# Kernel tuning notes

Measured on AMD Instinct MI355X. Metric: run time of the kernel, lower is better.

## Reference

```python
import jax, jax.numpy as jnp
import numpy as np

C = 768            # config.channels
CH, CW = 16, 16    # coarse span shape for group 'screen'
N = CH * CW        # total coarse positions = 256
FH, FW, FP = 16, 16, 2
F = FH * FW * FP   # fine_total = 512
K = 4              # top4 sample mode
B = 1024           # sb


def _ln(x, g, b, eps=1e-5):
    m = jnp.mean(x, axis=-1, keepdims=True)
    v = jnp.mean((x - m) ** 2, axis=-1, keepdims=True)
    return (x - m) / jnp.sqrt(v + eps) * g + b


def _mlp3(x, W1, b1, W2, b2, W3, b3):
    h = jax.nn.gelu(x @ W1 + b1)
    h = jax.nn.gelu(h @ W2 + b2)
    return h @ W3 + b3


def setup_inputs() -> dict:
    key = jax.random.key(0)
    ks = jax.random.split(key, 16)

    def w(k, fan_in, shape):
        return jax.random.normal(k, shape, jnp.float32) * (1.0 / np.sqrt(fan_in))

    return {
        "x": jax.random.normal(ks[0], (B, C), jnp.float32),
        "g_in": jnp.ones((C,), jnp.float32),
        "b_in": jnp.zeros((C,), jnp.float32),
        # coarse head: C -> C -> C -> N
        "cW1": w(ks[1], C, (C, C)), "cb1": jnp.zeros((C,), jnp.float32),
        "cW2": w(ks[2], C, (C, C)), "cb2": jnp.zeros((C,), jnp.float32),
        "cW3": w(ks[3], C, (C, N)), "cb3": jnp.zeros((N,), jnp.float32),
        # coarse embedding
        "emb": jax.random.normal(ks[4], (N, C), jnp.float32),
        "g_e": jnp.ones((C,), jnp.float32),
        "b_e": jnp.zeros((C,), jnp.float32),
        # fine head: 2C -> C -> C -> F
        "fW1": w(ks[5], 2 * C, (2 * C, C)), "fb1": jnp.zeros((C,), jnp.float32),
        "fW2": w(ks[6], C, (C, C)), "fb2": jnp.zeros((C,), jnp.float32),
        "fW3": w(ks[7], C, (C, F)), "fb3": jnp.zeros((F,), jnp.float32),
        # no-op head
        "nW": w(ks[8], C, (C, 1)), "nb": jnp.zeros((1,), jnp.float32),
    }


def reference(x, g_in, b_in, cW1, cb1, cW2, cb2, cW3, cb3, emb, g_e, b_e,
              fW1, fb1, fW2, fb2, fW3, fb3, nW, nb):
    b = x.shape[0]
    xn = _ln(x, g_in, b_in)                                   # (b, C)
    no_op = xn @ nW + nb                                      # (b, 1)
    coarse = _mlp3(xn, cW1, cb1, cW2, cb2, cW3, cb3)          # (b, N)

    # top4 routing
    _, i = jax.lax.top_k(coarse, K)                           # (b, K) int32
    e = _ln(emb[i], g_e, b_e)                                 # (b, K, C)
    fine_in = jnp.concatenate(
        [jnp.broadcast_to(xn[:, None, :], (b, K, C)), e], axis=-1)  # (b, K, 2C)
    fine = _mlp3(fine_in, fW1, fb1, fW2, fb2, fW3, fb3)       # (b, K, F)

    log_f = jnp.log(jnp.float32(F))
    xfull = jnp.broadcast_to(coarse[:, :, None], (b, N, F)) - log_f  # (b, N, F)
    upd = fine + log_f - jax.nn.logsumexp(fine, axis=-1, keepdims=True)
    xfull = xfull.at[jnp.arange(b)[:, None], i].add(upd)      # scatter-combine

    # per-group permute: (b, ch, cw, fh, fw, fp) -> (b, ch, fh, cw, fw, fp)
    xg = xfull.reshape(b, CH, CW, FH, FW, FP)
    xg = jnp.transpose(xg, (0, 1, 3, 2, 4, 5)).reshape(b, -1)
    return jnp.concatenate([no_op, xg], axis=-1)              # (b, 1 + N*F)
```

## Files before the change

### kernel.cpp

```cpp
#include <hip/hip_runtime.h>
#include <hip/hip_bf16.h>
#include <math.h>

typedef unsigned short u16;
typedef unsigned int   u32;
typedef __attribute__((ext_vector_type(8))) short s16x8;
typedef __attribute__((ext_vector_type(4))) float f32x4;

#define CB 768
#define NB 256
#define FB 512
#define BATCH 1024
#define OUTC 131073
#define LOGF 6.2383246250395077f

__device__ __forceinline__ u16 f2bf(float f){
    u32 u = __float_as_uint(f);
    u32 r = u + 0x7FFFu + ((u >> 16) & 1u);
    return (u16)(r >> 16);
}
__device__ __forceinline__ float bf2f(u16 s){ return __uint_as_float(((u32)s) << 16); }
__device__ __forceinline__ bool probe_bf(const void* g){ return ((const u16*)g)[0] == 0x3F80u; }
__device__ __forceinline__ float loadraw(const void* p, size_t i, bool isbf){
    return isbf ? bf2f(((const u16*)p)[i]) : ((const float*)p)[i];
}
__device__ __forceinline__ void split3(float f, u16& h, u16& l, u16& q){
    h = f2bf(f); float r1 = f - bf2f(h);
    l = f2bf(r1); float r2 = r1 - bf2f(l);
    q = f2bf(r2);
}
__device__ __forceinline__ float gelu_f(float x){
    return 0.5f * x * (1.0f + tanhf(0.7978845608028654f * (x + 0.044715f * x * x * x)));
}
__device__ __forceinline__ f32x4 mfma16x16x32(s16x8 a, s16x8 b, f32x4 c){
    return __builtin_amdgcn_mfma_f32_16x16x32_bf16(a, b, c, 0, 0, 0);
}

__device__ __forceinline__ float blockReduce(float v, float* sb, bool domax){
    #pragma unroll
    for (int o = 32; o > 0; o >>= 1){
        float ov = __shfl_down(v, o, 64);
        v = domax ? fmaxf(v, ov) : (v + ov);
    }
    int w = threadIdx.x >> 6, lane = threadIdx.x & 63;
    if (lane == 0) sb[w] = v;
    __syncthreads();
    float r = domax ? fmaxf(fmaxf(sb[0], sb[1]), fmaxf(sb[2], sb[3]))
                    : (sb[0] + sb[1] + sb[2] + sb[3]);
    __syncthreads();
    return r;
}

struct TransDesc { const void* src; u16* dh; u16* dl; int K; int N; int start; int tilesX; };
struct TD6 { TransDesc d[6]; };

#define T_TRANS 3456
#define T_LNEND 4480
#define T_CIEND 4496
#define T_GRID  4497

__global__ __launch_bounds__(256) void prep_k(TD6 td,
        const void* x, const void* g, const void* bb, const void* nW, const void* nb,
        const void* cb3, const void* ginp,
        u16* __restrict__ xh, u16* __restrict__ xl, u16* __restrict__ xq,
        float* __restrict__ noop, float* __restrict__ coarse, float* __restrict__ sumexp){
    __shared__ float t[32][33];
    __shared__ float sb[4];
    bool isbf = probe_bf(ginp);
    int blk = blockIdx.x, tid = threadIdx.x;
    if (blk < T_TRANS){
        int e = 0;
        #pragma unroll
        for (int i = 1; i < 6; i++) if (blk >= td.d[i].start) e = i;
        TransDesc d = td.d[e];
        int rel = blk - d.start;
        int n0 = (rel % d.tilesX) * 32;
        int k0 = (rel / d.tilesX) * 32;
        int tx = tid & 31, ty = tid >> 5;
        #pragma unroll
        for (int i = 0; i < 32; i += 8)
            t[ty + i][tx] = loadraw(d.src, (size_t)(k0 + ty + i) * d.N + n0 + tx, isbf);
        __syncthreads();
        #pragma unroll
        for (int i = 0; i < 32; i += 8){
            float f = t[tx][ty + i];
            u16 h = f2bf(f);
            d.dh[(size_t)(n0 + ty + i) * d.K + k0 + tx] = h;
            if (d.dl)
                d.dl[(size_t)(n0 + ty + i) * d.K + k0 + tx] = f2bf(f - bf2f(h));
        }
    } else if (blk < T_LNEND){
        int b = blk - T_TRANS;
        float v[3];
        #pragma unroll
        for (int i = 0; i < 3; i++) v[i] = loadraw(x, (size_t)b * CB + tid + i * 256, isbf);
        float mean = blockReduce(v[0] + v[1] + v[2], sb, false) * (1.0f / 768.0f);
        float d0 = v[0] - mean, d1 = v[1] - mean, d2 = v[2] - mean;
        float var = blockReduce(d0*d0 + d1*d1 + d2*d2, sb, false) * (1.0f / 768.0f);
        float inv = 1.0f / sqrtf(var + 1e-5f);
        float dot = 0.0f;
        #pragma unroll
        for (int i = 0; i < 3; i++){
            int c = tid + i * 256;
            float xi = (v[i] - mean) * inv * loadraw(g, c, isbf) + loadraw(bb, c, isbf);
            u16 h, l, q; split3(xi, h, l, q);
            size_t o = (size_t)b * CB + c;
            xh[o] = h; xl[o] = l; xq[o] = q;
            dot += xi * loadraw(nW, c, isbf);
        }
        dot = blockReduce(dot, sb, false);
        if (tid == 0) noop[b] = dot + loadraw(nb, 0, isbf);
    } else if (blk < T_CIEND){
        int base = (blk - T_LNEND) * 16384;
        #pragma unroll
        for (int j = 0; j < 64; j++){
            int i = base + j * 256 + tid;
            coarse[i] = loadraw(cb3, i & 255, isbf);
        }
    } else {
        #pragma unroll
        for (int j = 0; j < 16; j++) sumexp[j * 256 + tid] = 0.0f;
    }
}

template<int ASPLIT, int BSPLIT, int ACT, int OUTMODE, int TM, int TN>
__global__ __launch_bounds__(256) void gemm_k(
        const u16* __restrict__ Ah, const u16* __restrict__ Al, const u16* __restrict__ Aq,
        const u16* __restrict__ Bth, const u16* __restrict__ Btl,
        const void* __restrict__ bias, const void* __restrict__ ginp,
        void* __restrict__ o0, void* __restrict__ o1, void* __restrict__ o2,
        int M, int N, int K){
    constexpr int LDA = 40;
    constexpr int MT = TM / 32;
    constexpr int NT = TN / 32;
    constexpr int APT = (TM == 128) ? 2 : 1;
    constexpr int BPT = (TN == 128) ? 2 : 1;
    __shared__ u16 As[ASPLIT][TM * LDA];
    __shared__ u16 Bs[BSPLIT][TN * LDA];
    bool isbf = probe_bf(ginp);
    const int m0 = blockIdx.y * TM, n0 = blockIdx.x * TN;
    const int tid = threadIdx.x;
    const int w = tid >> 6, lane = tid & 63, lm = lane & 15, q = lane >> 4;
    const int wr = w & 1, wc = w >> 1;
    const int kc = K / gridDim.z;
    const int kbeg = blockIdx.z * kc, kend = kbeg + kc;
    f32x4 acc[MT][NT];
    #pragma unroll
    for (int i = 0; i < MT; i++)
        #pragma unroll
        for (int j = 0; j < NT; j++) acc[i][j] = (f32x4)(0.0f);
    const int ar = (TM == 128) ? (tid >> 1) : (tid >> 2);
    const int ac = (TM == 128) ? ((tid & 1) * 16) : ((tid & 3) * 8);
    const int bn = (TN == 128) ? (tid >> 1) : (tid >> 2);
    const int bc = (TN == 128) ? ((tid & 1) * 16) : ((tid & 3) * 8);
    const u16* Apl[3] = { Ah, Al, Aq };
    const u16* Bpl[2] = { Bth, Btl };

    s16x8 pa[ASPLIT][APT], pb[BSPLIT][BPT];
    auto load_regs = [&](int kk){
        #pragma unroll
        for (int s = 0; s < ASPLIT; s++){
            const u16* sp = Apl[s] + (size_t)(m0 + ar) * K + kk + ac;
            pa[s][0] = *(const s16x8*)(sp);
            if (APT == 2) pa[s][1] = *(const s16x8*)(sp + 8);
        }
        #pragma unroll
        for (int s = 0; s < BSPLIT; s++){
            const u16* sp = Bpl[s] + (size_t)(n0 + bn) * K + kk + bc;
            pb[s][0] = *(const s16x8*)(sp);
            if (BPT == 2) pb[s][1] = *(const s16x8*)(sp + 8);
        }
    };

    load_regs(kbeg);
    for (int k0 = kbeg; k0 < kend; k0 += 32){
        __syncthreads();
        #pragma unroll
        for (int s = 0; s < ASPLIT; s++){
            *(s16x8*)&As[s][ar*LDA + ac] = pa[s][0];
            if (APT == 2) *(s16x8*)&As[s][ar*LDA + ac + 8] = pa[s][1];
        }
        #pragma unroll
        for (int s = 0; s < BSPLIT; s++){
            *(s16x8*)&Bs[s][bn*LDA + bc] = pb[s][0];
            if (BPT == 2) *(s16x8*)&Bs[s][bn*LDA + bc + 8] = pb[s][1];
        }
        __syncthreads();
        if (k0 + 32 < kend) load_regs(k0 + 32);

        s16x8 afr[ASPLIT][MT], bfr[BSPLIT][NT];
        #pragma unroll
        for (int mt = 0; mt < MT; mt++)
            #pragma unroll
            for (int s = 0; s < ASPLIT; s++)
                afr[s][mt] = *(const s16x8*)&As[s][((mt*2 + wr)*16 + lm)*LDA + q*8];
        #pragma unroll
        for (int nt = 0; nt < NT; nt++)
            #pragma unroll
            for (int s = 0; s < BSPLIT; s++)
                bfr[s][nt] = *(const s16x8*)&Bs[s][((nt*2 + wc)*16 + lm)*LDA + q*8];
        #pragma unroll
        for (int mt = 0; mt < MT; mt++)
            #pragma unroll
            for (int nt = 0; nt < NT; nt++){
                acc[mt][nt] = mfma16x16x32(afr[0][mt], bfr[0][nt], acc[mt][nt]);
                if (ASPLIT == 3){
                    acc[mt][nt] = mfma16x16x32(afr[1][mt], bfr[0][nt], acc[mt][nt]);
                    acc[mt][nt] = mfma16x16x32(afr[2][mt], bfr[0][nt], acc[mt][nt]);
                }
                if (BSPLIT == 2){
                    acc[mt][nt] = mfma16x16x32(afr[0][mt], bfr[1][nt], acc[mt][nt]);
                    if (ASPLIT == 3)
                        acc[mt][nt] = mfma16x16x32(afr[1][mt], bfr[1][nt], acc[mt][nt]);
                }
            }
    }

    if (OUTMODE == 3){
        #pragma unroll
        for (int nt = 0; nt < NT; nt++){
            int n = n0 + (nt*2 + wc)*16 + lm;
            #pragma unroll
            for (int mt = 0; mt < MT; mt++)
                #pragma unroll
                for (int r = 0; r < 4; r++){
                    int m = m0 + (mt*2 + wr)*16 + q*4 + r;
                    atomicAdd(&((float*)o0)[(size_t)m * N + n], acc[mt][nt][r]);
                }
        }
    } else if (OUTMODE == 4){
        #pragma unroll
        for (int mt = 0; mt < MT; mt++)
            #pragma unroll
            for (int r = 0; r < 4; r++){
                int m = m0 + (mt*2 + wr)*16 + q*4 + r;
                float esum = 0.0f;
                #pragma unroll
                for (int nt = 0; nt < NT; nt++){
                    int n = n0 + (nt*2 + wc)*16 + lm;
                    float vv = acc[mt][nt][r] + loadraw(bias, n, isbf);
                    ((float*)o0)[(size_t)m * N + n] = vv;
                    esum += expf(vv);
                }
                #pragma unroll
                for (int o = 8; o > 0; o >>= 1) esum += __shfl_down(esum, o, 16);
                if (lm == 0) atomicAdd(&((float*)o1)[m], esum);
            }
    } else {
        #pragma unroll
        for (int nt = 0; nt < NT; nt++){
            int n = n0 + (nt*2 + wc)*16 + lm;
            float bv = loadraw(bias, n, isbf);
            #pragma unroll
            for (int mt = 0; mt < MT; mt++){
                #pragma unroll
                for (int r = 0; r < 4; r++){
                    int m = m0 + (mt*2 + wr)*16 + q*4 + r;
                    float vv = acc[mt][nt][r] + bv;
                    if (ACT == 1) vv = gelu_f(vv);
                    size_t o = (size_t)m * N + n;
                    if (OUTMODE == 0)      ((float*)o0)[o] = vv;
                    else if (OUTMODE == 1) ((u16*)o0)[o] = f2bf(vv);
                    else {
                        u16 h, l, qq; split3(vv, h, l, qq);
                        ((u16*)o0)[o] = h; ((u16*)o1)[o] = l; ((u16*)o2)[o] = qq;
                    }
                }
            }
        }
    }
}

__global__ __launch_bounds__(256) void topkfine_k(const float* __restrict__ coarse,
        const void* __restrict__ emb, const void* __restrict__ ge, const void* __restrict__ be,
        const void* __restrict__ ginp, const u16* __restrict__ xh,
        u16* __restrict__ fin, unsigned char* __restrict__ ksel){
    __shared__ float sb[4];
    __shared__ float swv[4]; __shared__ int swi[4];
    __shared__ int sel4[4]; __shared__ int chosen_s;
    bool isbf = probe_bf(ginp);
    int bk = blockIdx.x, tid = threadIdx.x;
    int b = bk >> 2, kk = bk & 3;
    int w = tid >> 6, lane = tid & 63;
    float v = coarse[(size_t)b * NB + tid];
    if (kk == 0) ksel[(size_t)b * NB + tid] = (unsigned char)255;
    __syncthreads();
    for (int k = 0; k < 4; k++){
        float bv = v; int bi = tid;
        #pragma unroll
        for (int o = 32; o > 0; o >>= 1){
            float ov = __shfl_xor(bv, o, 64);
            int   oi = __shfl_xor(bi, o, 64);
            if (ov > bv || (ov == bv && oi < bi)){ bv = ov; bi = oi; }
        }
        if (lane == 0){ swv[w] = bv; swi[w] = bi; }
        __syncthreads();
        if (tid == 0){
            float cv = swv[0]; int ci = swi[0];
            #pragma unroll
            for (int j = 1; j < 4; j++)
                if (swv[j] > cv || (swv[j] == cv && swi[j] < ci)){ cv = swv[j]; ci = swi[j]; }
            sel4[k] = ci; chosen_s = ci;
        }
        __syncthreads();
        if (tid == chosen_s) v = -INFINITY;
    }
    if (kk == 0 && tid == 0){
        #pragma unroll
        for (int j = 0; j < 4; j++) ksel[(size_t)b * NB + sel4[j]] = (unsigned char)j;
    }
    int n = sel4[kk];
    float vv[3];
    #pragma unroll
    for (int i = 0; i < 3; i++) vv[i] = loadraw(emb, (size_t)n * CB + tid + i * 256, isbf);
    float mean = blockReduce(vv[0] + vv[1] + vv[2], sb, false) * (1.0f / 768.0f);
    float d0 = vv[0] - mean, d1 = vv[1] - mean, d2 = vv[2] - mean;
    float var = blockReduce(d0*d0 + d1*d1 + d2*d2, sb, false) * (1.0f / 768.0f);
    float inv = 1.0f / sqrtf(var + 1e-5f);
    u16* dst = fin + ((size_t)b * 4 + kk) * (2 * CB);
    #pragma unroll
    for (int i = 0; i < 3; i++){
        int c = tid + i * 256;
        dst[c] = xh[(size_t)b * CB + c];
        dst[CB + c] = f2bf((vv[i] - mean) * inv * loadraw(ge, c, isbf) + loadraw(be, c, isbf));
    }
}

__global__ __launch_bounds__(256) void out_k(const float* __restrict__ coarse,
        const float* __restrict__ fine, const float* __restrict__ sumexp,
        const unsigned char* __restrict__ ksel, const float* __restrict__ noop,
        const void* __restrict__ ginp, void* __restrict__ outp){
    u32 g0 = ((u32)blockIdx.x * 256u + (u32)threadIdx.x) * 8u;
    const u32 total = (u32)BATCH * (u32)OUTC;
    if (g0 >= total) return;
    bool isbf = probe_bf(ginp);
    float vals[8];
    #pragma unroll
    for (int e = 0; e < 8; e++){
        u32 gg = g0 + (u32)e;
        u32 qq = gg >> 17;
        int rr = (int)(gg & 131071u) - (int)qq;
        if (rr < 0){ qq -= 1u; rr += 131073; }
        int b = (int)qq;
        float val;
        if (rr == 0){
            val = noop[b];
        } else {
            int j = rr - 1;
            int ch = j >> 13;
            int rem = j & 8191;
            int fh = rem >> 9, cw = (rem >> 5) & 15, ff = rem & 31;
            int n = (ch << 4) + cw;
            val = coarse[(size_t)b * NB + n] - LOGF;
            int ks = ksel[(size_t)b * NB + n];
            if (ks != 255){
                int fr = b * 4 + ks;
                val += fine[((size_t)fr << 9) + (fh << 5) + ff] + (LOGF - logf(sumexp[fr]));
            }
        }
        vals[e] = val;
    }
    if (isbf){
        u16 res[8];
        #pragma unroll
        for (int e = 0; e < 8; e++) res[e] = f2bf(vals[e]);
        *(s16x8*)((u16*)outp + g0) = *(s16x8*)res;
    } else {
        float* of = (float*)outp + g0;
        *(float4*)(of)     = make_float4(vals[0], vals[1], vals[2], vals[3]);
        *(float4*)(of + 4) = make_float4(vals[4], vals[5], vals[6], vals[7]);
    }
}

extern "C" void kernel_launch(void* const* d_in, const int* in_sizes, int n_in,
                              void* d_out, int out_size, void* d_ws, size_t ws_size,
                              hipStream_t stream){
    (void)in_sizes; (void)n_in; (void)out_size; (void)ws_size;
    char* ws = (char*)d_ws;
    size_t off = 0;
    auto alloc = [&](size_t bytes){ void* p = ws + off; off += (bytes + 255) & ~(size_t)255; return p; };

    u16* xh  = (u16*)alloc((size_t)1024*768*2);
    u16* xl  = (u16*)alloc((size_t)1024*768*2);
    u16* xq  = (u16*)alloc((size_t)1024*768*2);
    u16* h1h = (u16*)alloc((size_t)1024*768*2);
    u16* h1l = (u16*)alloc((size_t)1024*768*2);
    u16* h1q = (u16*)alloc((size_t)1024*768*2);
    u16* h2h = (u16*)alloc((size_t)1024*768*2);
    u16* h2l = (u16*)alloc((size_t)1024*768*2);
    u16* h2q = (u16*)alloc((size_t)1024*768*2);
    float* coarse = (float*)alloc((size_t)1024*256*4);
    unsigned char* ksel = (unsigned char*)alloc((size_t)1024*256);
    float* noop   = (float*)alloc((size_t)1024*4);
    float* sumexp = (float*)alloc((size_t)4096*4);
    u16*   fin    = (u16*)  alloc((size_t)4096*1536*2);
    u16*   gg1    = (u16*)  alloc((size_t)4096*768*2);
    u16*   gg2    = (u16*)  alloc((size_t)4096*768*2);
    float* fine   = (float*)alloc((size_t)4096*512*4);
    u16* cW1th = (u16*)alloc((size_t)768*768*2);
    u16* cW1tl = (u16*)alloc((size_t)768*768*2);
    u16* cW2th = (u16*)alloc((size_t)768*768*2);
    u16* cW2tl = (u16*)alloc((size_t)768*768*2);
    u16* cW3th = (u16*)alloc((size_t)768*256*2);
    u16* cW3tl = (u16*)alloc((size_t)768*256*2);
    u16* fW1t  = (u16*)alloc((size_t)1536*768*2);
    u16* fW2t  = (u16*)alloc((size_t)768*768*2);
    u16* fW3t  = (u16*)alloc((size_t)768*512*2);

    const void* ginp = d_in[1];

    TD6 td;
    td.d[0] = { d_in[3],  cW1th, cW1tl,  768, 768,    0, 24 };
    td.d[1] = { d_in[5],  cW2th, cW2tl,  768, 768,  576, 24 };
    td.d[2] = { d_in[7],  cW3th, cW3tl,  768, 256, 1152,  8 };
    td.d[3] = { d_in[12], fW1t,  nullptr,1536, 768, 1344, 24 };
    td.d[4] = { d_in[14], fW2t,  nullptr, 768, 768, 2496, 24 };
    td.d[5] = { d_in[16], fW3t,  nullptr, 768, 512, 3072, 16 };

    prep_k<<<T_GRID, 256, 0, stream>>>(td, d_in[0], d_in[1], d_in[2], d_in[18], d_in[19],
                                       d_in[8], ginp, xh, xl, xq, noop, coarse, sumexp);

    gemm_k<3,2,1,2,64,64><<<dim3(12, 16, 1), 256, 0, stream>>>(xh, xl, xq, cW1th, cW1tl,
            d_in[4], ginp, h1h, h1l, h1q, 1024, 768, 768);
    gemm_k<3,2,1,2,64,64><<<dim3(12, 16, 1), 256, 0, stream>>>(h1h, h1l, h1q, cW2th, cW2tl,
            d_in[6], ginp, h2h, h2l, h2q, 1024, 768, 768);
    gemm_k<3,2,0,3,64,64><<<dim3( 4, 16, 3), 256, 0, stream>>>(h2h, h2l, h2q, cW3th, cW3tl,
            nullptr, ginp, coarse, nullptr, nullptr, 1024, 256, 768);

    topkfine_k<<<4096, 256, 0, stream>>>(coarse, d_in[9], d_in[10], d_in[11], ginp, xh, fin, ksel);

    gemm_k<1,1,1,1,128,128><<<dim3(6, 32, 1), 256, 0, stream>>>(fin, nullptr, nullptr, fW1t, nullptr,
            d_in[13], ginp, gg1, nullptr, nullptr, 4096, 768, 1536);
    gemm_k<1,1,1,1,128,128><<<dim3(6, 32, 1), 256, 0, stream>>>(gg1, nullptr, nullptr, fW2t, nullptr,
            d_in[15], ginp, gg2, nullptr, nullptr, 4096, 768, 768);
    gemm_k<1,1,0,4,128,64><<<dim3(8, 32, 1), 256, 0, stream>>>(gg2, nullptr, nullptr, fW3t, nullptr,
            d_in[17], ginp, fine, sumexp, nullptr, 4096, 512, 768);

    u32 total_chunks = ((u32)BATCH * (u32)OUTC) / 8u;
    u32 blocks = (total_chunks + 255u) / 256u;
    out_k<<<blocks, 256, 0, stream>>>(coarse, fine, sumexp, ksel, noop, ginp, d_out);
}
```

Baseline: 813.0 us.

## Split fine layer-1 GEMM into shared x part and gathered embedding part

The first fine-head GEMM over the concatenated [xn, LN(emb[i])] input is split algebraically. The xn half is computed once per batch row (1024 rows instead of 4096) into an fp32 partial. The embedding half runs as a gather-GEMM over a table of 256 pre-normalized embedding rows, and the partial is added in a new epilogue before GELU. This removes the per-(b,k) embedding layernorm and the materialized concatenated input. Top-k moves to a lighter wave-per-row kernel, ksel initialization moves into the prep kernel, and the fine layer-3 tile changes to 128x128. The cost is an extra GEMM launch and the fp32 partial buffer traffic.

```diff
diff --git a/kernel.cpp b/kernel.cpp
--- a/kernel.cpp
+++ b/kernel.cpp
@@ -54,16 +54,20 @@
 struct TransDesc { const void* src; u16* dh; u16* dl; int K; int N; int start; int tilesX; };
 struct TD6 { TransDesc d[6]; };
 
-#define T_TRANS 3456
-#define T_LNEND 4480
-#define T_CIEND 4496
-#define T_GRID  4497
+#define T_TRANS   3456
+#define T_LNX_END 4480
+#define T_LEM_END 4736
+#define T_CI_END  4752
+#define T_KS_END  4768
+#define T_GRID    4769
 
 __global__ __launch_bounds__(256) void prep_k(TD6 td,
         const void* x, const void* g, const void* bb, const void* nW, const void* nb,
-        const void* cb3, const void* ginp,
+        const void* emb, const void* ge, const void* be, const void* cb3, const void* ginp,
         u16* __restrict__ xh, u16* __restrict__ xl, u16* __restrict__ xq,
-        float* __restrict__ noop, float* __restrict__ coarse, float* __restrict__ sumexp){
+        u16* __restrict__ lnemb, float* __restrict__ noop,
+        float* __restrict__ coarse, unsigned char* __restrict__ ksel,
+        float* __restrict__ sumexp){
     __shared__ float t[32][33];
     __shared__ float sb[4];
     bool isbf = probe_bf(ginp);
@@ -89,7 +93,7 @@
             if (d.dl)
                 d.dl[(size_t)(n0 + ty + i) * d.K + k0 + tx] = f2bf(f - bf2f(h));
         }
-    } else if (blk < T_LNEND){
+    } else if (blk < T_LNX_END){
         int b = blk - T_TRANS;
         float v[3];
         #pragma unroll
@@ -110,26 +114,47 @@
         }
         dot = blockReduce(dot, sb, false);
         if (tid == 0) noop[b] = dot + loadraw(nb, 0, isbf);
-    } else if (blk < T_CIEND){
-        int base = (blk - T_LNEND) * 16384;
+    } else if (blk < T_LEM_END){
+        int n = blk - T_LNX_END;
+        float v[3];
+        #pragma unroll
+        for (int i = 0; i < 3; i++) v[i] = loadraw(emb, (size_t)n * CB + tid + i * 256, isbf);
+        float mean = blockReduce(v[0] + v[1] + v[2], sb, false) * (1.0f / 768.0f);
+        float d0 = v[0] - mean, d1 = v[1] - mean, d2 = v[2] - mean;
+        float var = blockReduce(d0*d0 + d1*d1 + d2*d2, sb, false) * (1.0f / 768.0f);
+        float inv = 1.0f / sqrtf(var + 1e-5f);
+        #pragma unroll
+        for (int i = 0; i < 3; i++){
+            int c = tid + i * 256;
+            lnemb[(size_t)n * CB + c] =
+                f2bf((v[i] - mean) * inv * loadraw(ge, c, isbf) + loadraw(be, c, isbf));
+        }
+    } else if (blk < T_CI_END){
+        int base = (blk - T_LEM_END) * 16384;
         #pragma unroll
         for (int j = 0; j < 64; j++){
             int i = base + j * 256 + tid;
             coarse[i] = loadraw(cb3, i & 255, isbf);
         }
+    } else if (blk < T_KS_END){
+        int base = (blk - T_CI_END) * 4096;
+        u32* kp = (u32*)ksel;
+        #pragma unroll
+        for (int j = 0; j < 16; j++) kp[base + j * 256 + tid] = 0xFFFFFFFFu;
     } else {
         #pragma unroll
         for (int j = 0; j < 16; j++) sumexp[j * 256 + tid] = 0.0f;
     }
 }
 
-template<int ASPLIT, int BSPLIT, int ACT, int OUTMODE, int TM, int TN>
+template<int ASPLIT, int BSPLIT, int ACT, int OUTMODE, int TM, int TN, int GATHER>
 __global__ __launch_bounds__(256) void gemm_k(
         const u16* __restrict__ Ah, const u16* __restrict__ Al, const u16* __restrict__ Aq,
+        const int* __restrict__ gidx,
         const u16* __restrict__ Bth, const u16* __restrict__ Btl,
         const void* __restrict__ bias, const void* __restrict__ ginp,
         void* __restrict__ o0, void* __restrict__ o1, void* __restrict__ o2,
-        int M, int N, int K){
+        int M, int N, int K, int lda, int ldb){
     constexpr int LDA = 40;
     constexpr int MT = TM / 32;
     constexpr int NT = TN / 32;
@@ -155,18 +180,19 @@
     const int bc = (TN == 128) ? ((tid & 1) * 16) : ((tid & 3) * 8);
     const u16* Apl[3] = { Ah, Al, Aq };
     const u16* Bpl[2] = { Bth, Btl };
+    const int arow = GATHER ? gidx[m0 + ar] : (m0 + ar);
 
     s16x8 pa[ASPLIT][APT], pb[BSPLIT][BPT];
     auto load_regs = [&](int kk){
         #pragma unroll
         for (int s = 0; s < ASPLIT; s++){
-            const u16* sp = Apl[s] + (size_t)(m0 + ar) * K + kk + ac;
+            const u16* sp = Apl[s] + (size_t)arow * lda + kk + ac;
             pa[s][0] = *(const s16x8*)(sp);
             if (APT == 2) pa[s][1] = *(const s16x8*)(sp + 8);
         }
         #pragma unroll
         for (int s = 0; s < BSPLIT; s++){
-            const u16* sp = Bpl[s] + (size_t)(n0 + bn) * K + kk + bc;
+            const u16* sp = Bpl[s] + (size_t)(n0 + bn) * ldb + kk + bc;
             pb[s][0] = *(const s16x8*)(sp);
             if (BPT == 2) pb[s][1] = *(const s16x8*)(sp + 8);
         }
@@ -238,7 +264,7 @@
                 #pragma unroll
                 for (int nt = 0; nt < NT; nt++){
                     int n = n0 + (nt*2 + wc)*16 + lm;
-                    float vv = acc[mt][nt][r] + loadraw(bias, n, isbf);
+                    float vv = acc[mt][nt][r] + (bias ? loadraw(bias, n, isbf) : 0.0f);
                     ((float*)o0)[(size_t)m * N + n] = vv;
                     esum += expf(vv);
                 }
@@ -246,11 +272,26 @@
                 for (int o = 8; o > 0; o >>= 1) esum += __shfl_down(esum, o, 16);
                 if (lm == 0) atomicAdd(&((float*)o1)[m], esum);
             }
-    } else {
+    } else if (OUTMODE == 5){
         #pragma unroll
         for (int nt = 0; nt < NT; nt++){
             int n = n0 + (nt*2 + wc)*16 + lm;
-            float bv = loadraw(bias, n, isbf);
+            float bv = bias ? loadraw(bias, n, isbf) : 0.0f;
+            #pragma unroll
+            for (int mt = 0; mt < MT; mt++){
+                #pragma unroll
+                for (int r = 0; r < 4; r++){
+                    int m = m0 + (mt*2 + wr)*16 + q*4 + r;
+                    float xv = ((const float*)o1)[(size_t)(m >> 2) * N + n];
+                    ((u16*)o0)[(size_t)m * N + n] = f2bf(gelu_f(acc[mt][nt][r] + bv + xv));
+                }
+            }
+        }
+    } else {
+        #pragma unroll
+        for (int nt = 0; nt < NT; nt++){
+            int n = n0 + (nt*2 + wc)*16 + lm;
+            float bv = bias ? loadraw(bias, n, isbf) : 0.0f;
             #pragma unroll
             for (int mt = 0; mt < MT; mt++){
                 #pragma unroll
@@ -271,58 +312,28 @@
     }
 }
 
-__global__ __launch_bounds__(256) void topkfine_k(const float* __restrict__ coarse,
-        const void* __restrict__ emb, const void* __restrict__ ge, const void* __restrict__ be,
-        const void* __restrict__ ginp, const u16* __restrict__ xh,
-        u16* __restrict__ fin, unsigned char* __restrict__ ksel){
-    __shared__ float sb[4];
-    __shared__ float swv[4]; __shared__ int swi[4];
-    __shared__ int sel4[4]; __shared__ int chosen_s;
-    bool isbf = probe_bf(ginp);
-    int bk = blockIdx.x, tid = threadIdx.x;
-    int b = bk >> 2, kk = bk & 3;
-    int w = tid >> 6, lane = tid & 63;
-    float v = coarse[(size_t)b * NB + tid];
-    if (kk == 0) ksel[(size_t)b * NB + tid] = (unsigned char)255;
-    __syncthreads();
+__global__ __launch_bounds__(256) void topk_k(const float* __restrict__ coarse,
+        int* __restrict__ idx, unsigned char* __restrict__ ksel){
+    int w = threadIdx.x >> 6, lane = threadIdx.x & 63;
+    int b = blockIdx.x * 4 + w;
+    const float* cr = coarse + (size_t)b * NB;
+    float v[4]; int id[4];
+    #pragma unroll
+    for (int j = 0; j < 4; j++){ id[j] = lane + 64*j; v[j] = cr[id[j]]; }
     for (int k = 0; k < 4; k++){
-        float bv = v; int bi = tid;
+        float bv = v[0]; int bi = id[0];
+        #pragma unroll
+        for (int j = 1; j < 4; j++)
+            if (v[j] > bv || (v[j] == bv && id[j] < bi)){ bv = v[j]; bi = id[j]; }
         #pragma unroll
         for (int o = 32; o > 0; o >>= 1){
             float ov = __shfl_xor(bv, o, 64);
             int   oi = __shfl_xor(bi, o, 64);
             if (ov > bv || (ov == bv && oi < bi)){ bv = ov; bi = oi; }
         }
-        if (lane == 0){ swv[w] = bv; swi[w] = bi; }
-        __syncthreads();
-        if (tid == 0){
-            float cv = swv[0]; int ci = swi[0];
-            #pragma unroll
-            for (int j = 1; j < 4; j++)
-                if (swv[j] > cv || (swv[j] == cv && swi[j] < ci)){ cv = swv[j]; ci = swi[j]; }
-            sel4[k] = ci; chosen_s = ci;
-        }
-        __syncthreads();
-        if (tid == chosen_s) v = -INFINITY;
-    }
-    if (kk == 0 && tid == 0){
-        #pragma unroll
-        for (int j = 0; j < 4; j++) ksel[(size_t)b * NB + sel4[j]] = (unsigned char)j;
-    }
-    int n = sel4[kk];
-    float vv[3];
-    #pragma unroll
-    for (int i = 0; i < 3; i++) vv[i] = loadraw(emb, (size_t)n * CB + tid + i * 256, isbf);
-    float mean = blockReduce(vv[0] + vv[1] + vv[2], sb, false) * (1.0f / 768.0f);
-    float d0 = vv[0] - mean, d1 = vv[1] - mean, d2 = vv[2] - mean;
-    float var = blockReduce(d0*d0 + d1*d1 + d2*d2, sb, false) * (1.0f / 768.0f);
-    float inv = 1.0f / sqrtf(var + 1e-5f);
-    u16* dst = fin + ((size_t)b * 4 + kk) * (2 * CB);
-    #pragma unroll
-    for (int i = 0; i < 3; i++){
-        int c = tid + i * 256;
-        dst[c] = xh[(size_t)b * CB + c];
-        dst[CB + c] = f2bf((vv[i] - mean) * inv * loadraw(ge, c, isbf) + loadraw(be, c, isbf));
+        if (lane == 0){ idx[b*4 + k] = bi; ksel[(size_t)b * NB + bi] = (unsigned char)k; }
+        #pragma unroll
+        for (int j = 0; j < 4; j++) if (id[j] == bi) v[j] = -INFINITY;
     }
 }
 
@@ -389,11 +400,13 @@
     u16* h2h = (u16*)alloc((size_t)1024*768*2);
     u16* h2l = (u16*)alloc((size_t)1024*768*2);
     u16* h2q = (u16*)alloc((size_t)1024*768*2);
+    u16* lnemb = (u16*)alloc((size_t)256*768*2);
     float* coarse = (float*)alloc((size_t)1024*256*4);
     unsigned char* ksel = (unsigned char*)alloc((size_t)1024*256);
     float* noop   = (float*)alloc((size_t)1024*4);
     float* sumexp = (float*)alloc((size_t)4096*4);
-    u16*   fin    = (u16*)  alloc((size_t)4096*1536*2);
+    int*   idx    = (int*)alloc((size_t)4096*4);
+    float* xpart  = (float*)alloc((size_t)1024*768*4);
     u16*   gg1    = (u16*)  alloc((size_t)4096*768*2);
     u16*   gg2    = (u16*)  alloc((size_t)4096*768*2);
     float* fine   = (float*)alloc((size_t)4096*512*4);
@@ -403,9 +416,9 @@
     u16* cW2tl = (u16*)alloc((size_t)768*768*2);
     u16* cW3th = (u16*)alloc((size_t)768*256*2);
     u16* cW3tl = (u16*)alloc((size_t)768*256*2);
-    u16* fW1t  = (u16*)alloc((size_t)1536*768*2);
+    u16* fW1t  = (u16*)alloc((size_t)768*1536*2);
     u16* fW2t  = (u16*)alloc((size_t)768*768*2);
-    u16* fW3t  = (u16*)alloc((size_t)768*512*2);
+    u16* fW3t  = (u16*)alloc((size_t)512*768*2);
 
     const void* ginp = d_in[1];
 
@@ -418,23 +431,34 @@
     td.d[5] = { d_in[16], fW3t,  nullptr, 768, 512, 3072, 16 };
 
     prep_k<<<T_GRID, 256, 0, stream>>>(td, d_in[0], d_in[1], d_in[2], d_in[18], d_in[19],
-                                       d_in[8], ginp, xh, xl, xq, noop, coarse, sumexp);
-
-    gemm_k<3,2,1,2,64,64><<<dim3(12, 16, 1), 256, 0, stream>>>(xh, xl, xq, cW1th, cW1tl,
-            d_in[4], ginp, h1h, h1l, h1q, 1024, 768, 768);
-    gemm_k<3,2,1,2,64,64><<<dim3(12, 16, 1), 256, 0, stream>>>(h1h, h1l, h1q, cW2th, cW2tl,
-            d_in[6], ginp, h2h, h2l, h2q, 1024, 768, 768);
-    gemm_k<3,2,0,3,64,64><<<dim3( 4, 16, 3), 256, 0, stream>>>(h2h, h2l, h2q, cW3th, cW3tl,
-            nullptr, ginp, coarse, nullptr, nullptr, 1024, 256, 768);
-
-    topkfine_k<<<4096, 256, 0, stream>>>(coarse, d_in[9], d_in[10], d_in[11], ginp, xh, fin, ksel);
-
-    gemm_k<1,1,1,1,128,128><<<dim3(6, 32, 1), 256, 0, stream>>>(fin, nullptr, nullptr, fW1t, nullptr,
-            d_in[13], ginp, gg1, nullptr, nullptr, 4096, 768, 1536);
-    gemm_k<1,1,1,1,128,128><<<dim3(6, 32, 1), 256, 0, stream>>>(gg1, nullptr, nullptr, fW2t, nullptr,
-            d_in[15], ginp, gg2, nullptr, nullptr, 4096, 768, 768);
-    gemm_k<1,1,0,4,128,64><<<dim3(8, 32, 1), 256, 0, stream>>>(gg2, nullptr, nullptr, fW3t, nullptr,
-            d_in[17], ginp, fine, sumexp, nullptr, 4096, 512, 768);
+            d_in[9], d_in[10], d_in[11], d_in[8], ginp,
+            xh, xl, xq, lnemb, noop, coarse, ksel, sumexp);
+
+    gemm_k<1,1,0,0,128,128,0><<<dim3(6, 8, 1), 256, 0, stream>>>(
+            xh, nullptr, nullptr, nullptr, fW1t, nullptr,
+            nullptr, ginp, xpart, nullptr, nullptr, 1024, 768, 768, 768, 1536);
+
+    gemm_k<3,2,1,2,64,64,0><<<dim3(12, 16, 1), 256, 0, stream>>>(
+            xh, xl, xq, nullptr, cW1th, cW1tl,
+            d_in[4], ginp, h1h, h1l, h1q, 1024, 768, 768, 768, 768);
+    gemm_k<3,2,1,2,64,64,0><<<dim3(12, 16, 1), 256, 0, stream>>>(
+            h1h, h1l, h1q, nullptr, cW2th, cW2tl,
+            d_in[6], ginp, h2h, h2l, h2q, 1024, 768, 768, 768, 768);
+    gemm_k<3,2,0,3,64,64,0><<<dim3( 4, 16, 3), 256, 0, stream>>>(
+            h2h, h2l, h2q, nullptr, cW3th, cW3tl,
+            nullptr, ginp, coarse, nullptr, nullptr, 1024, 256, 768, 768, 768);
+
+    topk_k<<<256, 256, 0, stream>>>(coarse, idx, ksel);
+
+    gemm_k<1,1,0,5,128,128,1><<<dim3(6, 32, 1), 256, 0, stream>>>(
+            lnemb, nullptr, nullptr, idx, fW1t + 768, nullptr,
+            d_in[13], ginp, gg1, xpart, nullptr, 4096, 768, 768, 768, 1536);
+    gemm_k<1,1,1,1,128,128,0><<<dim3(6, 32, 1), 256, 0, stream>>>(
+            gg1, nullptr, nullptr, nullptr, fW2t, nullptr,
+            d_in[15], ginp, gg2, nullptr, nullptr, 4096, 768, 768, 768, 768);
+    gemm_k<1,1,0,4,128,128,0><<<dim3(4, 32, 1), 256, 0, stream>>>(
+            gg2, nullptr, nullptr, nullptr, fW3t, nullptr,
+            d_in[17], ginp, fine, sumexp, nullptr, 4096, 512, 768, 768, 768);
 
     u32 total_chunks = ((u32)BATCH * (u32)OUTC) / 8u;
     u32 blocks = (total_chunks + 255u) / 256u;
```

Result: no change. 807.5 us (-0.7%).
